# Kernel tuning notes

Hardware: AMD Instinct MI355X
Metric: run time of the kernel (lower is better)

The kernel has to match this reference:

```python
import jax, jax.numpy as jnp
import numpy as np

N, E, D, L = 32768, 65536, 128, 8

def setup_inputs() -> dict:
    key = jax.random.key(0)
    ks = jax.random.split(key, 32)
    def rn(i, shape, s=0.05):
        return jax.random.normal(ks[i], shape, dtype=jnp.float32) * s
    inp = dict(
        hs_init=rn(0, (N, D), 1.0),
        edge_index=jax.random.randint(ks[1], (2, E), 0, N, dtype=jnp.int32),
        gate=jax.random.randint(ks[2], (N,), 0, 3, dtype=jnp.int32),
        level=jax.random.randint(ks[3], (N,), 0, L + 1, dtype=jnp.int32),
        gcn_w=rn(4, (D, D)), gcn_b=rn(5, (D,)),
        mu_w=rn(6, (D, D)), mu_b=rn(7, (D,)),
        ls_w=rn(8, (D, D)), ls_b=rn(9, (D,)),
        as_w=rn(10, (D, D)), as_b=rn(11, (D,)),
        ns_w=rn(12, (D, D)), ns_b=rn(13, (D,)),
        af_w=rn(14, (2 * D, D)), af_b=rn(15, (D,)),
        nf_w=rn(16, (D, D)), nf_b=rn(17, (D,)),
        ua_w=rn(18, (2 * D, D)), ua_b=rn(19, (D,)),
        un_w=rn(20, (D, D)), un_b=rn(21, (D,)),
        dec_ws=rn(22, (D, D)), dec_wt=rn(23, (D, D)),
    )
    return inp

def reference(hs_init, edge_index, gate, level, gcn_w, gcn_b, mu_w, mu_b, ls_w, ls_b,
              as_w, as_b, ns_w, ns_b, af_w, af_b, nf_w, nf_b, ua_w, ua_b, un_w, un_b,
              dec_ws, dec_wt):
    seg = jax.ops.segment_sum
    src, dst = edge_index[0], edge_index[1]
    n = hs_init.shape[0]
    hs = hs_init                       # structural embedding [N, D]
    hf = jnp.zeros_like(hs)            # functional embedding [N, D]
    and_mask = gate == 1
    not_mask = gate == 2
    # --- GCN encoder (self-loops, symmetric in-degree normalization) ---
    x = hs @ gcn_w
    deg = seg(jnp.ones_like(src, dtype=x.dtype), dst, num_segments=n) + 1.0
    dis = jax.lax.rsqrt(deg)
    coef = (dis[src] * dis[dst])[:, None]
    x = seg(coef * x[src], dst, num_segments=n) + (1.0 / deg)[:, None] * x + gcn_b
    # --- VAE head: eval mode -> hs = mu (logstd computed as in module, unused) ---
    mu = x @ mu_w + mu_b
    logstd = jnp.minimum(x @ ls_w + ls_b, 10.0)  # MAX_LOGSTD clamp, eval-mode unused
    hs = mu
    # --- level-wise propagation: gather -> MLP aggr (sum) -> masked scatter update ---
    for l in range(1, L + 1):
        lvl = level == l
        # AND gates at this level
        m_and = and_mask & lvl
        e_and = m_and[dst].astype(hs.dtype)[:, None]   # edges targeting level-l ANDs
        msg = jax.nn.relu(hs @ as_w + as_b)
        agg = seg(e_and * msg[src], dst, num_segments=n)
        hs_and = jax.nn.relu(jnp.concatenate([hs, agg], axis=1) @ ua_w + ua_b)
        hs = jnp.where(m_and[:, None], hs_and, hs)
        fmsg = jax.nn.relu(jnp.concatenate([hs, hf], axis=1) @ af_w + af_b)
        fagg = seg(e_and * fmsg[src], dst, num_segments=n)
        hf = jnp.where(m_and[:, None], fagg, hf)
        # NOT gates at this level
        m_not = not_mask & lvl
        e_not = m_not[dst].astype(hs.dtype)[:, None]
        msg = jax.nn.relu(hs @ ns_w + ns_b)
        agg = seg(e_not * msg[src], dst, num_segments=n)
        hs_not = jnp.tanh(agg @ un_w + un_b)
        hs = jnp.where(m_not[:, None], hs_not, hs)
        fmsg = jax.nn.relu(hf @ nf_w + nf_b)
        fagg = seg(e_not * fmsg[src], dst, num_segments=n)
        hf = jnp.where(m_not[:, None], fagg, hf)
    # --- directed inner-product decoder -> node-level functional embedding ---
    zs = hs @ dec_ws
    zt = hs @ dec_wt
    w = jax.nn.sigmoid(jnp.sum(zs[src] * zt[dst], axis=-1))[:, None]  # [E,1]
    hf = seg(w * zs[src], dst, num_segments=n)
    return hs, hf
```

## Files before the change

### kernel.cpp

```cpp
#include <hip/hip_runtime.h>

#define DIM 128
#define NLEV 8
#define NB_STAGE 512
#define NSLOT (NB_STAGE * 4)
#define CAP (2 * NSLOT)

#define AS_OFF 0
#define UA_OFF 8192
#define NS_OFF 24576
#define UN_OFF 32768
#define PACK_TOTAL 40960

__device__ __forceinline__ int cls_of(int g, int l) {
    if (l < 1 || l > NLEV) return -1;
    if (g == 1) return l - 1;
    if (g == 2) return NLEV + (l - 1);
    return -1;
}


__global__ void deg_count_kernel(const int* __restrict__ dstv, int* __restrict__ degi, int E) {
    int i = blockIdx.x * blockDim.x + threadIdx.x;
    if (i < E) atomicAdd(&degi[dstv[i]], 1);
}

__global__ void pack_kernel(const float* __restrict__ as_w, const float* __restrict__ ua_w,
                            const float* __restrict__ ns_w, const float* __restrict__ un_w,
                            float2* __restrict__ wpack) {
    int i = blockIdx.x * 256 + threadIdx.x;
    if (i >= PACK_TOTAL) return;
    const float* src;
    int local;
    if (i < UA_OFF)      { src = as_w; local = i; }
    else if (i < NS_OFF) { src = ua_w; local = i - UA_OFF; }
    else if (i < UN_OFF) { src = ns_w; local = i - NS_OFF; }
    else                 { src = un_w; local = i - UN_OFF; }
    int k = local >> 6, jl = local & 63;
    wpack[i] = make_float2(src[k * DIM + jl], src[k * DIM + jl + 64]);
}

__global__ __launch_bounds__(DIM) void bprime_kernel(const float* __restrict__ gcn_b,
                                                     const float* __restrict__ mu_w,
                                                     const float* __restrict__ mu_b,
                                                     float* __restrict__ bp) {
    const int j = threadIdx.x;
    float acc = mu_b[j];
    for (int k = 0; k < DIM; k++) acc = fmaf(gcn_b[k], mu_w[k * DIM + j], acc);
    bp[j] = acc;
}

__global__ __launch_bounds__(1024) void scan1_kernel(const int* __restrict__ degi,
                                                     int* __restrict__ offs,
                                                     int* __restrict__ bsum,
                                                     float* __restrict__ dis,
                                                     float* __restrict__ inv) {
    __shared__ int sh[1024];
    const int gid = blockIdx.x * 1024 + threadIdx.x;
    const int v = degi[gid];
    {
        float d = (float)v + 1.0f;
        dis[gid] = rsqrtf(d);
        inv[gid] = 1.0f / d;
    }
    sh[threadIdx.x] = v;
    __syncthreads();
    for (int off = 1; off < 1024; off <<= 1) {
        int t = (threadIdx.x >= off) ? sh[threadIdx.x - off] : 0;
        __syncthreads();
        sh[threadIdx.x] += t;
        __syncthreads();
    }
    offs[gid] = sh[threadIdx.x] - v;
    if (threadIdx.x == 1023) bsum[blockIdx.x] = sh[1023];
}

__global__ void scan2_kernel(int* __restrict__ bsum, int nb) {
    const int lane = threadIdx.x & 63;
    const int orig = (lane < nb) ? bsum[lane] : 0;
    int v = orig;
#pragma unroll
    for (int off = 1; off < 64; off <<= 1) {
        int t = __shfl_up(v, off, 64);
        if (lane >= off) v += t;
    }
    if (lane < nb) bsum[lane] = v - orig;
    if (lane == nb - 1) bsum[nb] = v;
}

__global__ __launch_bounds__(1024) void scan3_kernel(int* __restrict__ offs,
                                                     const int* __restrict__ bsum, int n) {
    const int gid = blockIdx.x * 1024 + threadIdx.x;
    offs[gid] += bsum[blockIdx.x];
    if (gid == n - 1) offs[n] = bsum[gridDim.x];
}

__global__ void csr_fill_kernel(const int* __restrict__ srcv, const int* __restrict__ dstv,
                                const int* __restrict__ offs, int* __restrict__ cursor,
                                int* __restrict__ csr_src, int E) {
    int i = blockIdx.x * blockDim.x + threadIdx.x;
    if (i >= E) return;
    int d = dstv[i];
    int pos = offs[d] + atomicAdd(&cursor[d], 1);
    csr_src[pos] = srcv[i];
}

__global__ __launch_bounds__(256) void build_node_lists_kernel(const int* __restrict__ gate,
                                                               const int* __restrict__ level,
                                                               int* __restrict__ nlist,
                                                               int* __restrict__ ncnt,
                                                               int* __restrict__ clsidx, int n) {
    __shared__ int lcnt[16];
    __shared__ int lbase[16];
    int t = threadIdx.x;
    int i = blockIdx.x * 256 + t;
    if (t < 16) lcnt[t] = 0;
    __syncthreads();
    int c = -1, lpos = 0;
    if (i < n) {
        c = cls_of(gate[i], level[i]);
        if (c >= 0) lpos = atomicAdd(&lcnt[c], 1);
    }
    __syncthreads();
    if (t < 16 && lcnt[t] > 0) lbase[t] = atomicAdd(&ncnt[t], lcnt[t]);
    __syncthreads();
    if (c >= 0) {
        int idx = lbase[c] + lpos;
        nlist[c * n + idx] = i;
        clsidx[i] = (c << 16) | idx;
    }
}

template <int BIAS>
__global__ __launch_bounds__(256) void mm_kernel(const float* __restrict__ in0,
                                                 const float* __restrict__ W,
                                                 const float* __restrict__ b,
                                                 float* __restrict__ out, int n) {
    const int R = 32;
    __shared__ float tile[R * DIM];
    const size_t row0 = (size_t)blockIdx.x * R;
    for (int t = threadIdx.x; t < R * DIM / 4; t += 256)
        ((float4*)tile)[t] = ((const float4*)(in0 + row0 * DIM))[t];
    __syncthreads();
    const int g = threadIdx.x >> 7;
    const int j = threadIdx.x & 127;
    float acc[16];
#pragma unroll
    for (int r = 0; r < 16; r++) acc[r] = 0.f;
    const float* tb = tile + (g * 16) * DIM;
    for (int k = 0; k < DIM; k += 4) {
        float w0 = W[(k + 0) * DIM + j];
        float w1 = W[(k + 1) * DIM + j];
        float w2 = W[(k + 2) * DIM + j];
        float w3 = W[(k + 3) * DIM + j];
#pragma unroll
        for (int r = 0; r < 16; r++) {
            const float4 a = *reinterpret_cast<const float4*>(tb + r * DIM + k);
            acc[r] = fmaf(a.x, w0, acc[r]);
            acc[r] = fmaf(a.y, w1, acc[r]);
            acc[r] = fmaf(a.z, w2, acc[r]);
            acc[r] = fmaf(a.w, w3, acc[r]);
        }
    }
    float bias = BIAS ? b[j] : 0.f;
#pragma unroll
    for (int r = 0; r < 16; r++) out[(row0 + g * 16 + r) * DIM + j] = acc[r] + bias;
}

__global__ __launch_bounds__(256) void mm2_kernel(const float* __restrict__ in0,
                                                  const float* __restrict__ Ws,
                                                  const float* __restrict__ Wt,
                                                  float* __restrict__ zs,
                                                  float* __restrict__ zt, int n) {
    const int R = 32;
    __shared__ float tile[R * DIM];
    const size_t row0 = (size_t)blockIdx.x * R;
    for (int t = threadIdx.x; t < R * DIM / 4; t += 256)
        ((float4*)tile)[t] = ((const float4*)(in0 + row0 * DIM))[t];
    __syncthreads();
    const int g = threadIdx.x >> 7;
    const int j = threadIdx.x & 127;
    float accs[16], acct[16];
#pragma unroll
    for (int r = 0; r < 16; r++) { accs[r] = 0.f; acct[r] = 0.f; }
    const float* tb = tile + (g * 16) * DIM;
    for (int k = 0; k < DIM; k += 2) {
        float s0 = Ws[(k + 0) * DIM + j];
        float s1 = Ws[(k + 1) * DIM + j];
        float t0 = Wt[(k + 0) * DIM + j];
        float t1 = Wt[(k + 1) * DIM + j];
#pragma unroll
        for (int r = 0; r < 16; r++) {
            const float2 a = *reinterpret_cast<const float2*>(tb + r * DIM + k);
            accs[r] = fmaf(a.x, s0, accs[r]);
            accs[r] = fmaf(a.y, s1, accs[r]);
            acct[r] = fmaf(a.x, t0, acct[r]);
            acct[r] = fmaf(a.y, t1, acct[r]);
        }
    }
#pragma unroll
    for (int r = 0; r < 16; r++) {
        zs[(row0 + g * 16 + r) * DIM + j] = accs[r];
        zt[(row0 + g * 16 + r) * DIM + j] = acct[r];
    }
}

__global__ __launch_bounds__(256) void gcn_gather_kernel(const float* __restrict__ x,
                                                         const float* __restrict__ dis,
                                                         const float* __restrict__ inv,
                                                         const int* __restrict__ offs,
                                                         const int* __restrict__ csr_src,
                                                         float* __restrict__ y, int n) {
    int slot = threadIdx.x >> 7, j = threadIdx.x & 127;
    for (int node = blockIdx.x * 2 + slot; node < n; node += gridDim.x * 2) {
        float di = dis[node];
        float acc = inv[node] * x[(size_t)node * DIM + j];
        int e1 = offs[node + 1];
        for (int p = offs[node]; p < e1; p++) {
            int s = csr_src[p];
            acc += di * dis[s] * x[(size_t)s * DIM + j];
        }
        y[(size_t)node * DIM + j] = acc;
    }
}


__device__ __forceinline__ void stage_pk(const float2* __restrict__ Wp, float2* __restrict__ W2) {
    const float4* s = (const float4*)Wp;
    float4* d = (float4*)W2;
    for (int t = threadIdx.x; t < 4096; t += 256) d[t] = s[t];
}

template <bool MERGE>
__device__ __forceinline__ const float* resolve_row(const float* __restrict__ base,
                                                    const float* __restrict__ tmp,
                                                    const int* __restrict__ clsidx,
                                                    int mcls, int s) {
    if (MERGE) {
        int cc = clsidx[s];
        if ((cc >> 16) == mcls && (cc & 0xFFFF) < CAP) return tmp + (size_t)(cc & 0xFFFF) * DIM;
    }
    return base + (size_t)s * DIM;
}

template <bool MERGE>
__device__ __forceinline__ void load_pair(const float* __restrict__ hs,
                                          const float* __restrict__ tmp,
                                          const int* __restrict__ clsidx, int mcls,
                                          const int* __restrict__ csr_src,
                                          int p, int e1, int lane,
                                          float& a00, float& a01, float& a10, float& a11) {
    const int s0 = csr_src[p];
    const int s1 = (p + 1 < e1) ? csr_src[p + 1] : s0;
    const float* r0 = resolve_row<MERGE>(hs, tmp, clsidx, mcls, s0);
    const float* r1 = resolve_row<MERGE>(hs, tmp, clsidx, mcls, s1);
    a00 = r0[lane]; a01 = r0[lane + 64];
    a10 = r1[lane]; a11 = r1[lane + 64];
}

__device__ __forceinline__ void mv128(const float* __restrict__ ar, const float2* __restrict__ W2,
                                      int lane, float& o0, float& o1) {
#pragma unroll 8
    for (int k = 0; k < 128; k += 4) {
        const float4 a = *(const float4*)&ar[k];
        float2 w;
        w = W2[(k + 0) * 64 + lane]; o0 = fmaf(a.x, w.x, o0); o1 = fmaf(a.x, w.y, o1);
        w = W2[(k + 1) * 64 + lane]; o0 = fmaf(a.y, w.x, o0); o1 = fmaf(a.y, w.y, o1);
        w = W2[(k + 2) * 64 + lane]; o0 = fmaf(a.z, w.x, o0); o1 = fmaf(a.z, w.y, o1);
        w = W2[(k + 3) * 64 + lane]; o0 = fmaf(a.w, w.x, o0); o1 = fmaf(a.w, w.y, o1);
    }
}

template <bool MERGE>
__global__ __launch_bounds__(256) void and_stage_kernel(
        float* __restrict__ hs, const float* __restrict__ tmpN, float* __restrict__ tmpA,
        const int* __restrict__ offs, const int* __restrict__ csr_src,
        const int* __restrict__ nlist, const int* __restrict__ ncnt,
        const int* __restrict__ clsidx, const float2* __restrict__ wpack,
        const float* __restrict__ as_b, const float* __restrict__ ua_b,
        int cA, int cNp, int n) {
    const int cnt = min(ncnt[cA], CAP);
    const int cntp = MERGE ? min(ncnt[cNp], CAP) : 0;
    const int lim = max(cnt, cntp);
    if ((int)blockIdx.x * 4 >= lim) return;
    __shared__ float2 W2[128 * 64];
    __shared__ float arow[4][2][256];
    const int lane = threadIdx.x & 63;
    const int wv = threadIdx.x >> 6;
    const int gslot = (blockIdx.x << 2) | wv;

    bool act[2]; int nd[2], e0[2], e1[2];
#pragma unroll
    for (int it = 0; it < 2; it++) {
        const int idx = gslot + it * NSLOT;
        act[it] = idx < cnt;
        nd[it] = act[it] ? nlist[cA * n + idx] : 0;
        e0[it] = act[it] ? offs[nd[it]] : 0;
        e1[it] = act[it] ? offs[nd[it] + 1] : 0;
    }
    float h0[2] = {0.f, 0.f}, h1[2] = {0.f, 0.f};
#pragma unroll
    for (int it = 0; it < 2; it++) {
        if (act[it]) {
            h0[it] = hs[(size_t)nd[it] * DIM + lane];
            h1[it] = hs[(size_t)nd[it] * DIM + lane + 64];
        }
    }
    float pa[2][4];
#pragma unroll
    for (int it = 0; it < 2; it++) {
        if (act[it] && e0[it] < e1[it])
            load_pair<MERGE>(hs, tmpN, clsidx, cNp, csr_src, e0[it], e1[it], lane,
                             pa[it][0], pa[it][1], pa[it][2], pa[it][3]);
    }
    if (MERGE) {
        for (int idx = gslot; idx < cntp; idx += NSLOT) {
            const int node = nlist[cNp * n + idx];
            hs[(size_t)node * DIM + lane] = tmpN[(size_t)idx * DIM + lane];
            hs[(size_t)node * DIM + lane + 64] = tmpN[(size_t)idx * DIM + lane + 64];
        }
    }
    stage_pk(wpack + AS_OFF, W2);
    __syncthreads();

    const float bj_as0 = as_b[lane], bj_as1 = as_b[lane + 64];
    float ag0[2] = {0.f, 0.f}, ag1[2] = {0.f, 0.f};
#pragma unroll
    for (int it = 0; it < 2; it++) {
        if (!act[it]) continue;
        float* ar = arow[wv][it];
        float a00 = pa[it][0], a01 = pa[it][1], a10 = pa[it][2], a11 = pa[it][3];
        for (int p = e0[it]; p < e1[it]; p += 2) {
            ar[lane] = a00; ar[64 + lane] = a01;
            ar[128 + lane] = a10; ar[192 + lane] = a11;
            const bool two = (p + 1 < e1[it]);
            float n00 = 0.f, n01 = 0.f, n10 = 0.f, n11 = 0.f;
            if (p + 2 < e1[it])
                load_pair<MERGE>(hs, tmpN, clsidx, cNp, csr_src, p + 2, e1[it], lane,
                                 n00, n01, n10, n11);
            float m00 = bj_as0, m01 = bj_as1, m10 = bj_as0, m11 = bj_as1;
#pragma unroll 8
            for (int k = 0; k < 128; k += 4) {
                const float4 a0 = *(const float4*)&ar[k];
                const float4 a1 = *(const float4*)&ar[128 + k];
                float2 w;
                w = W2[(k + 0) * 64 + lane];
                m00 = fmaf(a0.x, w.x, m00); m01 = fmaf(a0.x, w.y, m01);
                m10 = fmaf(a1.x, w.x, m10); m11 = fmaf(a1.x, w.y, m11);
                w = W2[(k + 1) * 64 + lane];
                m00 = fmaf(a0.y, w.x, m00); m01 = fmaf(a0.y, w.y, m01);
                m10 = fmaf(a1.y, w.x, m10); m11 = fmaf(a1.y, w.y, m11);
                w = W2[(k + 2) * 64 + lane];
                m00 = fmaf(a0.z, w.x, m00); m01 = fmaf(a0.z, w.y, m01);
                m10 = fmaf(a1.z, w.x, m10); m11 = fmaf(a1.z, w.y, m11);
                w = W2[(k + 3) * 64 + lane];
                m00 = fmaf(a0.w, w.x, m00); m01 = fmaf(a0.w, w.y, m01);
                m10 = fmaf(a1.w, w.x, m10); m11 = fmaf(a1.w, w.y, m11);
            }
            ag0[it] += fmaxf(m00, 0.f);
            ag1[it] += fmaxf(m01, 0.f);
            if (two) { ag0[it] += fmaxf(m10, 0.f); ag1[it] += fmaxf(m11, 0.f); }
            a00 = n00; a01 = n01; a10 = n10; a11 = n11;
        }
    }

    float u0[2], u1[2];
    u0[0] = ua_b[lane]; u1[0] = ua_b[lane + 64];
    u0[1] = u0[0]; u1[1] = u1[0];
    __syncthreads();
    stage_pk(wpack + UA_OFF, W2);
    __syncthreads();
#pragma unroll
    for (int it = 0; it < 2; it++) {
        if (!act[it]) continue;
        float* ar = arow[wv][it];
        ar[lane] = h0[it]; ar[64 + lane] = h1[it];
        mv128(ar, W2, lane, u0[it], u1[it]);
    }
    __syncthreads();
    stage_pk(wpack + UA_OFF + 8192, W2);
    __syncthreads();
#pragma unroll
    for (int it = 0; it < 2; it++) {
        if (!act[it]) continue;
        float* ar = arow[wv][it];
        ar[lane] = ag0[it]; ar[64 + lane] = ag1[it];
        mv128(ar, W2, lane, u0[it], u1[it]);
        const int idx = gslot + it * NSLOT;
        tmpA[(size_t)idx * DIM + lane] = fmaxf(u0[it], 0.f);
        tmpA[(size_t)idx * DIM + lane + 64] = fmaxf(u1[it], 0.f);
    }
}

__global__ __launch_bounds__(256) void not_stage_kernel(
        float* __restrict__ hs, const float* __restrict__ tmpA, float* __restrict__ tmpN,
        const int* __restrict__ offs, const int* __restrict__ csr_src,
        const int* __restrict__ nlist, const int* __restrict__ ncnt,
        const int* __restrict__ clsidx, const float2* __restrict__ wpack,
        const float* __restrict__ ns_b, const float* __restrict__ un_b,
        int cA, int cN, int n) {
    const int cnt = min(ncnt[cN], CAP);
    const int cntA = min(ncnt[cA], CAP);
    const int lim = max(cnt, cntA);
    if ((int)blockIdx.x * 4 >= lim) return;
    __shared__ float2 W2[128 * 64];
    __shared__ float arow[4][2][256];
    const int lane = threadIdx.x & 63;
    const int wv = threadIdx.x >> 6;
    const int gslot = (blockIdx.x << 2) | wv;

    bool act[2]; int nd[2], e0[2], e1[2];
#pragma unroll
    for (int it = 0; it < 2; it++) {
        const int idx = gslot + it * NSLOT;
        act[it] = idx < cnt;
        nd[it] = act[it] ? nlist[cN * n + idx] : 0;
        e0[it] = act[it] ? offs[nd[it]] : 0;
        e1[it] = act[it] ? offs[nd[it] + 1] : 0;
    }
    float pa[2][4];
#pragma unroll
    for (int it = 0; it < 2; it++) {
        if (act[it] && e0[it] < e1[it])
            load_pair<true>(hs, tmpA, clsidx, cA, csr_src, e0[it], e1[it], lane,
                            pa[it][0], pa[it][1], pa[it][2], pa[it][3]);
    }
    for (int idx = gslot; idx < cntA; idx += NSLOT) {
        const int node = nlist[cA * n + idx];
        hs[(size_t)node * DIM + lane] = tmpA[(size_t)idx * DIM + lane];
        hs[(size_t)node * DIM + lane + 64] = tmpA[(size_t)idx * DIM + lane + 64];
    }
    stage_pk(wpack + NS_OFF, W2);
    __syncthreads();

    const float bj_ns0 = ns_b[lane], bj_ns1 = ns_b[lane + 64];
    float ag0[2] = {0.f, 0.f}, ag1[2] = {0.f, 0.f};
#pragma unroll
    for (int it = 0; it < 2; it++) {
        if (!act[it]) continue;
        float* ar = arow[wv][it];
        float a00 = pa[it][0], a01 = pa[it][1], a10 = pa[it][2], a11 = pa[it][3];
        for (int p = e0[it]; p < e1[it]; p += 2) {
            ar[lane] = a00; ar[64 + lane] = a01;
            ar[128 + lane] = a10; ar[192 + lane] = a11;
            const bool two = (p + 1 < e1[it]);
            float n00 = 0.f, n01 = 0.f, n10 = 0.f, n11 = 0.f;
            if (p + 2 < e1[it])
                load_pair<true>(hs, tmpA, clsidx, cA, csr_src, p + 2, e1[it], lane,
                                n00, n01, n10, n11);
            float m00 = bj_ns0, m01 = bj_ns1, m10 = bj_ns0, m11 = bj_ns1;
#pragma unroll 8
            for (int k = 0; k < 128; k += 4) {
                const float4 a0 = *(const float4*)&ar[k];
                const float4 a1 = *(const float4*)&ar[128 + k];
                float2 w;
                w = W2[(k + 0) * 64 + lane];
                m00 = fmaf(a0.x, w.x, m00); m01 = fmaf(a0.x, w.y, m01);
                m10 = fmaf(a1.x, w.x, m10); m11 = fmaf(a1.x, w.y, m11);
                w = W2[(k + 1) * 64 + lane];
                m00 = fmaf(a0.y, w.x, m00); m01 = fmaf(a0.y, w.y, m01);
                m10 = fmaf(a1.y, w.x, m10); m11 = fmaf(a1.y, w.y, m11);
                w = W2[(k + 2) * 64 + lane];
                m00 = fmaf(a0.z, w.x, m00); m01 = fmaf(a0.z, w.y, m01);
                m10 = fmaf(a1.z, w.x, m10); m11 = fmaf(a1.z, w.y, m11);
                w = W2[(k + 3) * 64 + lane];
                m00 = fmaf(a0.w, w.x, m00); m01 = fmaf(a0.w, w.y, m01);
                m10 = fmaf(a1.w, w.x, m10); m11 = fmaf(a1.w, w.y, m11);
            }
            ag0[it] += fmaxf(m00, 0.f);
            ag1[it] += fmaxf(m01, 0.f);
            if (two) { ag0[it] += fmaxf(m10, 0.f); ag1[it] += fmaxf(m11, 0.f); }
            a00 = n00; a01 = n01; a10 = n10; a11 = n11;
        }
    }

    float u0[2], u1[2];
    u0[0] = un_b[lane]; u1[0] = un_b[lane + 64];
    u0[1] = u0[0]; u1[1] = u1[0];
    __syncthreads();
    stage_pk(wpack + UN_OFF, W2);
    __syncthreads();
#pragma unroll
    for (int it = 0; it < 2; it++) {
        if (!act[it]) continue;
        float* ar = arow[wv][it];
        ar[lane] = ag0[it]; ar[64 + lane] = ag1[it];
        mv128(ar, W2, lane, u0[it], u1[it]);
        const int idx = gslot + it * NSLOT;
        tmpN[(size_t)idx * DIM + lane] = tanhf(u0[it]);
        tmpN[(size_t)idx * DIM + lane + 64] = tanhf(u1[it]);
    }
}

__global__ __launch_bounds__(256) void commit_kernel(float* __restrict__ hs,
                                                     const float* __restrict__ tmp,
                                                     const int* __restrict__ nlist,
                                                     const int* __restrict__ ncnt,
                                                     int c, int n) {
    const int lane = threadIdx.x & 63;
    const int gslot = (blockIdx.x << 2) | (threadIdx.x >> 6);
    const int cnt = min(ncnt[c], CAP);
    for (int idx = gslot; idx < cnt; idx += NSLOT) {
        const int node = nlist[c * n + idx];
        hs[(size_t)node * DIM + lane] = tmp[(size_t)idx * DIM + lane];
        hs[(size_t)node * DIM + lane + 64] = tmp[(size_t)idx * DIM + lane + 64];
    }
}

__global__ __launch_bounds__(256) void dec_gather_kernel(const float* __restrict__ zs,
                                                         const float* __restrict__ zt,
                                                         const int* __restrict__ offs,
                                                         const int* __restrict__ csr_src,
                                                         float* __restrict__ hf_out, int n) {
    int w = threadIdx.x >> 6, lane = threadIdx.x & 63;
    for (int node = blockIdx.x * 4 + w; node < n; node += gridDim.x * 4) {
        float b0 = zt[(size_t)node * DIM + lane];
        float b1 = zt[(size_t)node * DIM + 64 + lane];
        float acc0 = 0.f, acc1 = 0.f;
        int e1 = offs[node + 1];
        for (int p = offs[node]; p < e1; p++) {
            int s = csr_src[p];
            float a0 = zs[(size_t)s * DIM + lane];
            float a1 = zs[(size_t)s * DIM + 64 + lane];
            float pd = a0 * b0 + a1 * b1;
#pragma unroll
            for (int off = 32; off > 0; off >>= 1) pd += __shfl_xor(pd, off, 64);
            float wg = 1.f / (1.f + __expf(-pd));
            acc0 += wg * a0;
            acc1 += wg * a1;
        }
        hf_out[(size_t)node * DIM + lane] = acc0;
        hf_out[(size_t)node * DIM + 64 + lane] = acc1;
    }
}

extern "C" void kernel_launch(void* const* d_in, const int* in_sizes, int n_in,
                              void* d_out, int out_size, void* d_ws, size_t ws_size,
                              hipStream_t stream) {
    const float* hs_init = (const float*)d_in[0];
    const int* ei = (const int*)d_in[1];
    const int* gate = (const int*)d_in[2];
    const int* level = (const int*)d_in[3];
    const float* gcn_w = (const float*)d_in[4];
    const float* gcn_b = (const float*)d_in[5];
    const float* mu_w = (const float*)d_in[6];
    const float* mu_b = (const float*)d_in[7];
    const float* as_w = (const float*)d_in[10];
    const float* as_b = (const float*)d_in[11];
    const float* ns_w = (const float*)d_in[12];
    const float* ns_b = (const float*)d_in[13];
    const float* ua_w = (const float*)d_in[18];
    const float* ua_b = (const float*)d_in[19];
    const float* un_w = (const float*)d_in[20];
    const float* un_b = (const float*)d_in[21];
    const float* dec_ws_w = (const float*)d_in[22];
    const float* dec_wt_w = (const float*)d_in[23];

    const int n = in_sizes[0] / DIM;
    const int E = in_sizes[1] / 2;
    const int* srcv = ei;
    const int* dstv = ei + E;

    float* hs = (float*)d_out;
    float* hf_out = hs + (size_t)n * DIM;

    char* wp = (char*)d_ws;
    float* x = (float*)wp;      wp += (size_t)n * DIM * 4;
    float* x2 = (float*)wp;     wp += (size_t)n * DIM * 4;
    float* tmpA = (float*)wp;   wp += (size_t)CAP * DIM * 4;
    float* tmpN = (float*)wp;   wp += (size_t)CAP * DIM * 4;
    float2* wpack = (float2*)wp; wp += (size_t)PACK_TOTAL * 8;
    float* wprime = (float*)wp; wp += (size_t)DIM * DIM * 4;
    float* bprime = (float*)wp; wp += (size_t)DIM * 4;
    char* small0 = wp;
    int* degi = (int*)wp;   wp += (size_t)n * 4;
    int* cursor = (int*)wp; wp += (size_t)n * 4;
    int* ncnt = (int*)wp;   wp += 16 * 4;
    size_t small_bytes = (size_t)(wp - small0);
    int* bsum = (int*)wp;    wp += 64 * 4;
    int* offs = (int*)wp;    wp += (size_t)(n + 1) * 4;
    int* csr_src = (int*)wp; wp += (size_t)E * 4;
    int* nlist = (int*)wp;   wp += (size_t)16 * n * 4;
    int* clsidx = (int*)wp;  wp += (size_t)n * 4;
    float* dis = (float*)wp; wp += (size_t)n * 4;
    float* inv = (float*)wp; wp += (size_t)n * 4;

    hipMemsetAsync(small0, 0, small_bytes, stream);
    hipMemsetAsync(clsidx, 0xFF, (size_t)n * 4, stream);

    mm_kernel<0><<<DIM / 32, 256, 0, stream>>>(gcn_w, mu_w, nullptr, wprime, DIM);
    bprime_kernel<<<1, DIM, 0, stream>>>(gcn_b, mu_w, mu_b, bprime);
    pack_kernel<<<(PACK_TOTAL + 255) / 256, 256, 0, stream>>>(as_w, ua_w, ns_w, un_w, wpack);

    deg_count_kernel<<<(E + 255) / 256, 256, 0, stream>>>(dstv, degi, E);
    build_node_lists_kernel<<<(n + 255) / 256, 256, 0, stream>>>(gate, level, nlist, ncnt, clsidx, n);
    scan1_kernel<<<n / 1024, 1024, 0, stream>>>(degi, offs, bsum, dis, inv);
    scan2_kernel<<<1, 64, 0, stream>>>(bsum, n / 1024);
    scan3_kernel<<<n / 1024, 1024, 0, stream>>>(offs, bsum, n);
    csr_fill_kernel<<<(E + 255) / 256, 256, 0, stream>>>(srcv, dstv, offs, cursor, csr_src, E);

    gcn_gather_kernel<<<4096, 256, 0, stream>>>(hs_init, dis, inv, offs, csr_src, x, n);
    mm_kernel<1><<<n / 32, 256, 0, stream>>>(x, wprime, bprime, hs, n);

    for (int l = 1; l <= NLEV; l++) {
        const int cA = l - 1;
        const int cN = NLEV + l - 1;
        const int cNp = NLEV + l - 2;
        if (l == 1)
            and_stage_kernel<false><<<NB_STAGE, 256, 0, stream>>>(
                hs, tmpN, tmpA, offs, csr_src, nlist, ncnt, clsidx, wpack,
                as_b, ua_b, cA, -9, n);
        else
            and_stage_kernel<true><<<NB_STAGE, 256, 0, stream>>>(
                hs, tmpN, tmpA, offs, csr_src, nlist, ncnt, clsidx, wpack,
                as_b, ua_b, cA, cNp, n);
        not_stage_kernel<<<NB_STAGE, 256, 0, stream>>>(
            hs, tmpA, tmpN, offs, csr_src, nlist, ncnt, clsidx, wpack,
            ns_b, un_b, cA, cN, n);
    }
    commit_kernel<<<NB_STAGE, 256, 0, stream>>>(hs, tmpN, nlist, ncnt, 2 * NLEV - 1, n);

    float* zs = x;
    float* zt = x2;
    mm2_kernel<<<n / 32, 256, 0, stream>>>(hs, dec_ws_w, dec_wt_w, zs, zt, n);
    dec_gather_kernel<<<4096, 256, 0, stream>>>(zs, zt, offs, csr_src, hf_out, n);
}
```

Baseline: 502.8 us.

## Merge setup kernels and enlarge matmul row tiles with weight prefetch

Folds the bias-prime computation into the pack kernel, merges degree counting with node-list building, and moves the single-block bsum scan into each scan3 block, which removes three launches. Separately, the dense matmul kernels now process 64 rows per block instead of 32, and each loads the next k-step's weights one iteration ahead. The larger tiles double per-thread accumulators and shared memory, which may cut occupancy and halve the grid to 512 blocks. The count_kernel guards node-list work with blockIdx*256<n, which is safe because E exceeds n.

Measured after the change: 563.8 us. 1.12x slower.

```diff
diff --git a/kernel.cpp b/kernel.cpp
--- a/kernel.cpp
+++ b/kernel.cpp
@@ -20,14 +20,51 @@
 }
 
 
-__global__ void deg_count_kernel(const int* __restrict__ dstv, int* __restrict__ degi, int E) {
-    int i = blockIdx.x * blockDim.x + threadIdx.x;
+__global__ __launch_bounds__(256) void count_kernel(const int* __restrict__ dstv,
+                                                    int* __restrict__ degi, int E,
+                                                    const int* __restrict__ gate,
+                                                    const int* __restrict__ level,
+                                                    int* __restrict__ nlist,
+                                                    int* __restrict__ ncnt,
+                                                    int* __restrict__ clsidx, int n) {
+    const int i = blockIdx.x * 256 + threadIdx.x;
     if (i < E) atomicAdd(&degi[dstv[i]], 1);
+    if ((int)blockIdx.x * 256 < n) {
+        __shared__ int lcnt[16];
+        __shared__ int lbase[16];
+        const int t = threadIdx.x;
+        if (t < 16) lcnt[t] = 0;
+        __syncthreads();
+        int c = -1, lpos = 0;
+        if (i < n) {
+            c = cls_of(gate[i], level[i]);
+            if (c >= 0) lpos = atomicAdd(&lcnt[c], 1);
+        }
+        __syncthreads();
+        if (t < 16 && lcnt[t] > 0) lbase[t] = atomicAdd(&ncnt[t], lcnt[t]);
+        __syncthreads();
+        if (c >= 0) {
+            int idx = lbase[c] + lpos;
+            nlist[c * n + idx] = i;
+            clsidx[i] = (c << 16) | idx;
+        }
+    }
 }
 
 __global__ void pack_kernel(const float* __restrict__ as_w, const float* __restrict__ ua_w,
                             const float* __restrict__ ns_w, const float* __restrict__ un_w,
-                            float2* __restrict__ wpack) {
+                            float2* __restrict__ wpack,
+                            const float* __restrict__ gcn_b, const float* __restrict__ mu_w,
+                            const float* __restrict__ mu_b, float* __restrict__ bp) {
+    if (blockIdx.x == gridDim.x - 1) {
+        const int j = threadIdx.x;
+        if (j < DIM) {
+            float acc = mu_b[j];
+            for (int k = 0; k < DIM; k++) acc = fmaf(gcn_b[k], mu_w[k * DIM + j], acc);
+            bp[j] = acc;
+        }
+        return;
+    }
     int i = blockIdx.x * 256 + threadIdx.x;
     if (i >= PACK_TOTAL) return;
     const float* src;
@@ -38,16 +75,6 @@
     else                 { src = un_w; local = i - UN_OFF; }
     int k = local >> 6, jl = local & 63;
     wpack[i] = make_float2(src[k * DIM + jl], src[k * DIM + jl + 64]);
-}
-
-__global__ __launch_bounds__(DIM) void bprime_kernel(const float* __restrict__ gcn_b,
-                                                     const float* __restrict__ mu_w,
-                                                     const float* __restrict__ mu_b,
-                                                     float* __restrict__ bp) {
-    const int j = threadIdx.x;
-    float acc = mu_b[j];
-    for (int k = 0; k < DIM; k++) acc = fmaf(gcn_b[k], mu_w[k * DIM + j], acc);
-    bp[j] = acc;
 }
 
 __global__ __launch_bounds__(1024) void scan1_kernel(const int* __restrict__ degi,
@@ -75,24 +102,26 @@
     if (threadIdx.x == 1023) bsum[blockIdx.x] = sh[1023];
 }
 
-__global__ void scan2_kernel(int* __restrict__ bsum, int nb) {
-    const int lane = threadIdx.x & 63;
-    const int orig = (lane < nb) ? bsum[lane] : 0;
-    int v = orig;
-#pragma unroll
-    for (int off = 1; off < 64; off <<= 1) {
-        int t = __shfl_up(v, off, 64);
-        if (lane >= off) v += t;
-    }
-    if (lane < nb) bsum[lane] = v - orig;
-    if (lane == nb - 1) bsum[nb] = v;
-}
-
 __global__ __launch_bounds__(1024) void scan3_kernel(int* __restrict__ offs,
                                                      const int* __restrict__ bsum, int n) {
+    __shared__ int sbase, stot;
+    const int nb = gridDim.x;
+    if (threadIdx.x < 64) {
+        const int lane = threadIdx.x;
+        const int orig = (lane < nb) ? bsum[lane] : 0;
+        int v = orig;
+#pragma unroll
+        for (int off = 1; off < 64; off <<= 1) {
+            int t = __shfl_up(v, off, 64);
+            if (lane >= off) v += t;
+        }
+        if (lane == (int)blockIdx.x) sbase = v - orig;
+        if (lane == nb - 1) stot = v;
+    }
+    __syncthreads();
     const int gid = blockIdx.x * 1024 + threadIdx.x;
-    offs[gid] += bsum[blockIdx.x];
-    if (gid == n - 1) offs[n] = bsum[gridDim.x];
+    offs[gid] += sbase;
+    if (gid == n - 1) offs[n] = stot;
 }
 
 __global__ void csr_fill_kernel(const int* __restrict__ srcv, const int* __restrict__ dstv,
@@ -105,38 +134,12 @@
     csr_src[pos] = srcv[i];
 }
 
-__global__ __launch_bounds__(256) void build_node_lists_kernel(const int* __restrict__ gate,
-                                                               const int* __restrict__ level,
-                                                               int* __restrict__ nlist,
-                                                               int* __restrict__ ncnt,
-                                                               int* __restrict__ clsidx, int n) {
-    __shared__ int lcnt[16];
-    __shared__ int lbase[16];
-    int t = threadIdx.x;
-    int i = blockIdx.x * 256 + t;
-    if (t < 16) lcnt[t] = 0;
-    __syncthreads();
-    int c = -1, lpos = 0;
-    if (i < n) {
-        c = cls_of(gate[i], level[i]);
-        if (c >= 0) lpos = atomicAdd(&lcnt[c], 1);
-    }
-    __syncthreads();
-    if (t < 16 && lcnt[t] > 0) lbase[t] = atomicAdd(&ncnt[t], lcnt[t]);
-    __syncthreads();
-    if (c >= 0) {
-        int idx = lbase[c] + lpos;
-        nlist[c * n + idx] = i;
-        clsidx[i] = (c << 16) | idx;
-    }
-}
-
 template <int BIAS>
 __global__ __launch_bounds__(256) void mm_kernel(const float* __restrict__ in0,
                                                  const float* __restrict__ W,
                                                  const float* __restrict__ b,
                                                  float* __restrict__ out, int n) {
-    const int R = 32;
+    const int R = 64;
     __shared__ float tile[R * DIM];
     const size_t row0 = (size_t)blockIdx.x * R;
     for (int t = threadIdx.x; t < R * DIM / 4; t += 256)
@@ -144,27 +147,30 @@
     __syncthreads();
     const int g = threadIdx.x >> 7;
     const int j = threadIdx.x & 127;
-    float acc[16];
-#pragma unroll
-    for (int r = 0; r < 16; r++) acc[r] = 0.f;
-    const float* tb = tile + (g * 16) * DIM;
+    float acc[32];
+#pragma unroll
+    for (int r = 0; r < 32; r++) acc[r] = 0.f;
+    const float* tb = tile + (g * 32) * DIM;
+    float w0 = W[0 * DIM + j], w1 = W[1 * DIM + j], w2 = W[2 * DIM + j], w3 = W[3 * DIM + j];
     for (int k = 0; k < DIM; k += 4) {
-        float w0 = W[(k + 0) * DIM + j];
-        float w1 = W[(k + 1) * DIM + j];
-        float w2 = W[(k + 2) * DIM + j];
-        float w3 = W[(k + 3) * DIM + j];
-#pragma unroll
-        for (int r = 0; r < 16; r++) {
+        const int kn = (k + 4 < DIM) ? (k + 4) : 0;
+        const float nw0 = W[(kn + 0) * DIM + j];
+        const float nw1 = W[(kn + 1) * DIM + j];
+        const float nw2 = W[(kn + 2) * DIM + j];
+        const float nw3 = W[(kn + 3) * DIM + j];
+#pragma unroll
+        for (int r = 0; r < 32; r++) {
             const float4 a = *reinterpret_cast<const float4*>(tb + r * DIM + k);
             acc[r] = fmaf(a.x, w0, acc[r]);
             acc[r] = fmaf(a.y, w1, acc[r]);
             acc[r] = fmaf(a.z, w2, acc[r]);
             acc[r] = fmaf(a.w, w3, acc[r]);
         }
+        w0 = nw0; w1 = nw1; w2 = nw2; w3 = nw3;
     }
     float bias = BIAS ? b[j] : 0.f;
 #pragma unroll
-    for (int r = 0; r < 16; r++) out[(row0 + g * 16 + r) * DIM + j] = acc[r] + bias;
+    for (int r = 0; r < 32; r++) out[(row0 + g * 32 + r) * DIM + j] = acc[r] + bias;
 }
 
 __global__ __launch_bounds__(256) void mm2_kernel(const float* __restrict__ in0,
@@ -172,7 +178,7 @@
                                                   const float* __restrict__ Wt,
                                                   float* __restrict__ zs,
                                                   float* __restrict__ zt, int n) {
-    const int R = 32;
+    const int R = 64;
     __shared__ float tile[R * DIM];
     const size_t row0 = (size_t)blockIdx.x * R;
     for (int t = threadIdx.x; t < R * DIM / 4; t += 256)
@@ -180,28 +186,32 @@
     __syncthreads();
     const int g = threadIdx.x >> 7;
     const int j = threadIdx.x & 127;
-    float accs[16], acct[16];
-#pragma unroll
-    for (int r = 0; r < 16; r++) { accs[r] = 0.f; acct[r] = 0.f; }
-    const float* tb = tile + (g * 16) * DIM;
+    float accs[32], acct[32];
+#pragma unroll
+    for (int r = 0; r < 32; r++) { accs[r] = 0.f; acct[r] = 0.f; }
+    const float* tb = tile + (g * 32) * DIM;
+    float s0 = Ws[0 * DIM + j], s1 = Ws[1 * DIM + j];
+    float t0 = Wt[0 * DIM + j], t1 = Wt[1 * DIM + j];
     for (int k = 0; k < DIM; k += 2) {
-        float s0 = Ws[(k + 0) * DIM + j];
-        float s1 = Ws[(k + 1) * DIM + j];
-        float t0 = Wt[(k + 0) * DIM + j];
-        float t1 = Wt[(k + 1) * DIM + j];
-#pragma unroll
-        for (int r = 0; r < 16; r++) {
+        const int kn = (k + 2 < DIM) ? (k + 2) : 0;
+        const float ns0 = Ws[(kn + 0) * DIM + j];
+        const float ns1 = Ws[(kn + 1) * DIM + j];
+        const float nt0 = Wt[(kn + 0) * DIM + j];
+        const float nt1 = Wt[(kn + 1) * DIM + j];
+#pragma unroll
+        for (int r = 0; r < 32; r++) {
             const float2 a = *reinterpret_cast<const float2*>(tb + r * DIM + k);
             accs[r] = fmaf(a.x, s0, accs[r]);
             accs[r] = fmaf(a.y, s1, accs[r]);
             acct[r] = fmaf(a.x, t0, acct[r]);
             acct[r] = fmaf(a.y, t1, acct[r]);
         }
-    }
-#pragma unroll
-    for (int r = 0; r < 16; r++) {
-        zs[(row0 + g * 16 + r) * DIM + j] = accs[r];
-        zt[(row0 + g * 16 + r) * DIM + j] = acct[r];
+        s0 = ns0; s1 = ns1; t0 = nt0; t1 = nt1;
+    }
+#pragma unroll
+    for (int r = 0; r < 32; r++) {
+        zs[(row0 + g * 32 + r) * DIM + j] = accs[r];
+        zt[(row0 + g * 32 + r) * DIM + j] = acct[r];
     }
 }
 
@@ -588,19 +598,18 @@
     hipMemsetAsync(small0, 0, small_bytes, stream);
     hipMemsetAsync(clsidx, 0xFF, (size_t)n * 4, stream);
 
-    mm_kernel<0><<<DIM / 32, 256, 0, stream>>>(gcn_w, mu_w, nullptr, wprime, DIM);
-    bprime_kernel<<<1, DIM, 0, stream>>>(gcn_b, mu_w, mu_b, bprime);
-    pack_kernel<<<(PACK_TOTAL + 255) / 256, 256, 0, stream>>>(as_w, ua_w, ns_w, un_w, wpack);
-
-    deg_count_kernel<<<(E + 255) / 256, 256, 0, stream>>>(dstv, degi, E);
-    build_node_lists_kernel<<<(n + 255) / 256, 256, 0, stream>>>(gate, level, nlist, ncnt, clsidx, n);
+    mm_kernel<0><<<DIM / 64, 256, 0, stream>>>(gcn_w, mu_w, nullptr, wprime, DIM);
+    pack_kernel<<<(PACK_TOTAL + 255) / 256 + 1, 256, 0, stream>>>(as_w, ua_w, ns_w, un_w, wpack,
+                                                                  gcn_b, mu_w, mu_b, bprime);
+
+    count_kernel<<<(E + 255) / 256, 256, 0, stream>>>(dstv, degi, E, gate, level,
+                                                      nlist, ncnt, clsidx, n);
     scan1_kernel<<<n / 1024, 1024, 0, stream>>>(degi, offs, bsum, dis, inv);
-    scan2_kernel<<<1, 64, 0, stream>>>(bsum, n / 1024);
     scan3_kernel<<<n / 1024, 1024, 0, stream>>>(offs, bsum, n);
     csr_fill_kernel<<<(E + 255) / 256, 256, 0, stream>>>(srcv, dstv, offs, cursor, csr_src, E);
 
     gcn_gather_kernel<<<4096, 256, 0, stream>>>(hs_init, dis, inv, offs, csr_src, x, n);
-    mm_kernel<1><<<n / 32, 256, 0, stream>>>(x, wprime, bprime, hs, n);
+    mm_kernel<1><<<n / 64, 256, 0, stream>>>(x, wprime, bprime, hs, n);
 
     for (int l = 1; l <= NLEV; l++) {
         const int cA = l - 1;
@@ -622,6 +631,6 @@
 
     float* zs = x;
     float* zt = x2;
-    mm2_kernel<<<n / 32, 256, 0, stream>>>(hs, dec_ws_w, dec_wt_w, zs, zt, n);
+    mm2_kernel<<<n / 64, 256, 0, stream>>>(hs, dec_ws_w, dec_wt_w, zs, zt, n);
     dec_gather_kernel<<<4096, 256, 0, stream>>>(zs, zt, offs, csr_src, hf_out, n);
 }
```
